# Kernel optimization log

Hardware: AMD Instinct MI355X
Metric: run time of the kernel (lower is better)

## Reference

```python
import jax, jax.numpy as jnp
import numpy as np

HID = 50        # lstm hidden_dim (hardcoded by Linear(50,100) etc.)
HS = 165        # lstm input size = 100 + 46 + 19
FEAT = 100      # encoder feature dim of H
CQ = 50257      # countq (output vocab)
EXT = 1000      # extended (copy) vocab
L = 250000      # source length


def setup_inputs() -> dict:
    key = jax.random.key(0)
    ks = jax.random.split(key, 24)
    s = 0.05
    f32 = jnp.float32
    inp = {}
    inp["H"] = jax.random.normal(ks[0], (1, L, FEAT), f32)
    inp["y"] = jax.random.normal(ks[1], (HS,), f32)
    inp["h0"] = jax.random.normal(ks[2], (1, 1, HID), f32)
    inp["c0"] = jax.random.normal(ks[3], (1, 1, HID), f32)
    inp["cont"] = jax.random.randint(ks[4], (L,), 0, CQ + EXT, dtype=jnp.int32)
    inp["ext"] = EXT
    # LSTM params (PyTorch gate order: i, f, g, o)
    inp["W_ih"] = jax.random.normal(ks[5], (4 * HID, HS), f32) * s
    inp["W_hh"] = jax.random.normal(ks[6], (4 * HID, HID), f32) * s
    inp["b_ih"] = jax.random.normal(ks[7], (4 * HID,), f32) * s
    inp["b_hh"] = jax.random.normal(ks[8], (4 * HID,), f32) * s
    # Linear layers (torch weight layout [out, in])
    inp["w_h_W"] = jax.random.normal(ks[9], (FEAT, HID), f32) * s
    inp["w_h_b"] = jax.random.normal(ks[10], (FEAT,), f32) * s
    inp["l1_W"] = jax.random.normal(ks[11], (200, 150), f32) * s
    inp["l1_b"] = jax.random.normal(ks[12], (200,), f32) * s
    inp["l2_W"] = jax.random.normal(ks[13], (CQ, 200), f32) * s
    inp["l2_b"] = jax.random.normal(ks[14], (CQ,), f32) * s
    inp["l3_W"] = jax.random.normal(ks[15], (1, HID), f32) * s
    inp["l3_b"] = jax.random.normal(ks[16], (1,), f32) * s
    inp["l4_W"] = jax.random.normal(ks[17], (1, HID), f32) * s
    inp["l4_b"] = jax.random.normal(ks[18], (1,), f32) * s
    return inp


def reference(H, y, h0, c0, cont, ext, W_ih, W_hh, b_ih, b_hh,
              w_h_W, w_h_b, l1_W, l1_b, l2_W, l2_b, l3_W, l3_b, l4_W, l4_b):
    # --- single LSTM step (batch=1, layer=1) ---
    h_prev = h0[0, 0]                       # [HID]
    c_prev = c0[0, 0]                       # [HID]
    gates = W_ih @ y + b_ih + W_hh @ h_prev + b_hh   # [4*HID]
    i, f, g, o = jnp.split(gates, 4)
    i = jax.nn.sigmoid(i); f = jax.nn.sigmoid(f)
    g = jnp.tanh(g);       o = jax.nn.sigmoid(o)
    c_new = f * c_prev + i * g
    h_new = o * jnp.tanh(c_new)             # [HID]
    # --- attention over source ---
    q = w_h_W @ h_new + w_h_b               # [FEAT]
    a_t = jax.nn.softmax(H[0] @ q)          # [L]
    c_t = H[0].T @ a_t                      # [FEAT]
    # --- vocab distribution ---
    temp = jnp.concatenate([h_new, c_t], 0)         # [150]
    e_t = jax.nn.sigmoid(l1_W @ temp + l1_b)        # [200]
    out = l2_W @ e_t + l2_b                         # [CQ]
    out = jnp.concatenate([out, jnp.zeros((ext,), out.dtype)], 0)  # [CQ+ext]
    p1 = jax.nn.sigmoid(l3_W @ h_new + l3_b)[0]     # scalar
    p2 = jax.nn.sigmoid(l4_W @ h_new + l4_b)[0]     # scalar
    out = p1 * out
    attn = p2 * a_t                                  # [L]
    # pointer copy: scatter_add attention mass into extended vocab
    out = out.at[cont].add(attn)
    logp = jax.nn.log_softmax(out)[None, :]          # [1, CQ+ext]
    return logp, h_new[None, None, :], c_new[None, None, :]
```

## Files before the change

### kernel.cpp

```cpp
#include <hip/hip_runtime.h>
#include <math.h>

#define L 250000
#define FEAT 100
#define HID 50
#define HS 165
#define CQ 50257
#define EXTV 1000
#define NOUT (CQ + EXTV)

#define NBLK23 2048
#define NW23 (NBLK23 * 4)
#define NBLK5R ((NOUT + 63) / 64)
#define NCOL 101

#define WS_Q     0
#define WS_P1    100
#define WS_P2    101
#define WS_SCALE 102
#define WS_DENOM 103
#define WS_CT    104
#define WS_ET    204
#define WS_H     404
#define WS_LSE   454
#define WS_ADD   512
#define WS_OUT   51776
#define WS_MS    103040
#define WS_PT    104960

__device__ __forceinline__ float sigm(float x) { return 1.f / (1.f + expf(-x)); }

__global__ void k1_lstm(const float* __restrict__ y, const float* __restrict__ h0,
                        const float* __restrict__ c0,
                        const float* __restrict__ W_ih, const float* __restrict__ W_hh,
                        const float* __restrict__ b_ih, const float* __restrict__ b_hh,
                        const float* __restrict__ w_h_W, const float* __restrict__ w_h_b,
                        const float* __restrict__ l3_W, const float* __restrict__ l3_b,
                        const float* __restrict__ l4_W, const float* __restrict__ l4_b,
                        float* __restrict__ ws, float* __restrict__ out) {
    int t = threadIdx.x;
    if (blockIdx.x != 0) {
        float* add = ws + WS_ADD;
        for (int i = (blockIdx.x - 1) * 256 + t; i < NOUT; i += 63 * 256) add[i] = 0.f;
        return;
    }
    __shared__ float s_y[HS], s_h[HID], s_c[HID], s_g[4 * HID], s_hn[HID];
    if (t < HS) s_y[t] = y[t];
    if (t < HID) { s_h[t] = h0[t]; s_c[t] = c0[t]; }
    __syncthreads();
    if (t < 4 * HID) {
        float acc = b_ih[t] + b_hh[t];
        const float* wi = W_ih + t * HS;
        for (int k = 0; k < HS; ++k) acc += wi[k] * s_y[k];
        const float* wh = W_hh + t * HID;
        for (int k = 0; k < HID; ++k) acc += wh[k] * s_h[k];
        s_g[t] = acc;
    }
    __syncthreads();
    if (t < HID) {
        float ig = sigm(s_g[t]);
        float fg = sigm(s_g[HID + t]);
        float gg = tanhf(s_g[2 * HID + t]);
        float og = sigm(s_g[3 * HID + t]);
        float cn = fg * s_c[t] + ig * gg;
        float hn = og * tanhf(cn);
        s_hn[t] = hn;
        ws[WS_H + t] = hn;
        out[NOUT + t] = hn;
        out[NOUT + HID + t] = cn;
    }
    __syncthreads();
    if (t < FEAT) {
        float acc = w_h_b[t];
        const float* w = w_h_W + t * HID;
        for (int k = 0; k < HID; ++k) acc += w[k] * s_hn[k];
        ws[WS_Q + t] = acc;
    }
    if (t == 200) {
        float acc = l3_b[0];
        for (int k = 0; k < HID; ++k) acc += l3_W[k] * s_hn[k];
        ws[WS_P1] = sigm(acc);
    }
    if (t == 201) {
        float acc = l4_b[0];
        for (int k = 0; k < HID; ++k) acc += l4_W[k] * s_hn[k];
        ws[WS_P2] = sigm(acc);
    }
}

__global__ void __launch_bounds__(256, 8)
k23_fused(const float* __restrict__ H, const int* __restrict__ cont,
          float* __restrict__ ws, float* __restrict__ pt) {
    __shared__ float s_ct[4][FEAT];
    __shared__ float s_d[4];
    int t = threadIdx.x;
    int w = t >> 6, lane = t & 63;
    int l32 = lane & 31, half = lane >> 5;
    long wid = (long)blockIdx.x * 4 + w;
    long r0 = (wid * L) / NW23;
    long r1 = ((wid + 1) * L) / NW23;

    float q[4];
    q[0] = ws[WS_Q + l32];
    q[1] = ws[WS_Q + l32 + 32];
    q[2] = ws[WS_Q + l32 + 64];
    q[3] = (l32 < 4) ? ws[WS_Q + l32 + 96] : 0.f;

    float cacc[4] = {0.f, 0.f, 0.f, 0.f};
    float dacc = 0.f, my_e = 0.f;

    for (long r = r0; r < r1; r += 8) {
        float hh[4][4], pd[4];
#pragma unroll
        for (int p = 0; p < 4; ++p) {
            long row = r + 2 * p + half;
            if (row < r1) {
                const float* P = H + row * FEAT;
                hh[p][0] = P[l32];
                hh[p][1] = P[l32 + 32];
                hh[p][2] = P[l32 + 64];
                hh[p][3] = (l32 < 4) ? P[l32 + 96] : 0.f;
            } else {
                hh[p][0] = hh[p][1] = hh[p][2] = hh[p][3] = 0.f;
            }
        }
#pragma unroll
        for (int p = 0; p < 4; ++p)
            pd[p] = hh[p][0] * q[0] + hh[p][1] * q[1] + hh[p][2] * q[2] + hh[p][3] * q[3];
#pragma unroll
        for (int o = 1; o < 32; o <<= 1) {
#pragma unroll
            for (int p = 0; p < 4; ++p) pd[p] += __shfl_xor(pd[p], o);
        }
#pragma unroll
        for (int p = 0; p < 4; ++p) {
            float e = expf(pd[p]);
            float eo = __shfl_xor(e, 32);
            float eA = half ? eo : e;
            float eB = half ? e : eo;
            long rA = r + 2 * p, rB = rA + 1;
            if (rA < r1) {
                dacc += eA;
                my_e = ((int)(rA - r0) == lane) ? eA : my_e;
            }
            if (rB < r1) {
                dacc += eB;
                my_e = ((int)(rB - r0) == lane) ? eB : my_e;
            }
            cacc[0] += e * hh[p][0];
            cacc[1] += e * hh[p][1];
            cacc[2] += e * hh[p][2];
            cacc[3] += e * hh[p][3];
        }
    }
#pragma unroll
    for (int k = 0; k < 4; ++k) cacc[k] += __shfl_xor(cacc[k], 32);
    int cnt = (int)(r1 - r0);
    if (lane < cnt) {
        int c = cont[r0 + lane];
        atomicAdd(ws + WS_ADD + c, my_e);
    }
    if (half == 0) {
        s_ct[w][l32] = cacc[0];
        s_ct[w][l32 + 32] = cacc[1];
        s_ct[w][l32 + 64] = cacc[2];
        if (l32 < 4) s_ct[w][96 + l32] = cacc[3];
    }
    if (lane == 0) s_d[w] = dacc;
    __syncthreads();
    if (t < FEAT)
        pt[(size_t)t * NBLK23 + blockIdx.x] =
            s_ct[0][t] + s_ct[1][t] + s_ct[2][t] + s_ct[3][t];
    if (t == FEAT)
        pt[(size_t)FEAT * NBLK23 + blockIdx.x] = s_d[0] + s_d[1] + s_d[2] + s_d[3];
}

__global__ void k3r_reduce(const float* __restrict__ pt, float* __restrict__ ws) {
    __shared__ float sw[4];
    int col = blockIdx.x;
    int t = threadIdx.x;
    const float* p = pt + (size_t)col * NBLK23;
    float s = 0.f;
#pragma unroll
    for (int k = 0; k < NBLK23 / 256; ++k) s += p[t + k * 256];
#pragma unroll
    for (int o = 1; o < 64; o <<= 1) s += __shfl_xor(s, o);
    if ((t & 63) == 0) sw[t >> 6] = s;
    __syncthreads();
    if (t == 0) {
        float tot = sw[0] + sw[1] + sw[2] + sw[3];
        if (col < FEAT) ws[WS_CT + col] = tot;
        else ws[WS_DENOM] = tot;
    }
}

__global__ void k4_et(const float* __restrict__ l1_W, const float* __restrict__ l1_b,
                      float* __restrict__ ws) {
    __shared__ float s_t[152];
    int t = threadIdx.x;
    float denom = ws[WS_DENOM];
    if (t < HID) s_t[t] = ws[WS_H + t];
    if (t < FEAT) s_t[HID + t] = ws[WS_CT + t] / denom;
    if (t == 0) ws[WS_SCALE] = ws[WS_P2] / denom;
    __syncthreads();
    if (t < 200) {
        float acc = l1_b[t];
        const float* wv = l1_W + t * 150;
        for (int k = 0; k < 150; ++k) acc += wv[k] * s_t[k];
        ws[WS_ET + t] = sigm(acc);
    }
}

__global__ void __launch_bounds__(256)
k5_vocab(const float* __restrict__ l2_W, const float* __restrict__ l2_b,
         float* __restrict__ ws, float* __restrict__ outv) {
    __shared__ float4 s_e[50];
    __shared__ float s_ms[8];
    int t = threadIdx.x, w = t >> 6, lane = t & 63;
    if (t < 50) s_e[t] = ((const float4*)(ws + WS_ET))[t];
    __syncthreads();
    float p1 = ws[WS_P1], scale = ws[WS_SCALE];
    const float* add = ws + WS_ADD;
    int row = blockIdx.x * 64 + (t >> 2);
    int q = t & 3;
    float m = -1e30f, s = 0.f;
    float acc = 0.f;
    if (row < CQ) {
        const float4* wrow = (const float4*)l2_W + (size_t)row * 50;
        float4 a[13];
#pragma unroll
        for (int j = 0; j < 12; ++j) a[j] = wrow[q + 4 * j];
        a[12] = (q < 2) ? wrow[48 + q] : make_float4(0.f, 0.f, 0.f, 0.f);
#pragma unroll
        for (int j = 0; j < 12; ++j) {
            float4 b = s_e[q + 4 * j];
            acc += a[j].x * b.x + a[j].y * b.y + a[j].z * b.z + a[j].w * b.w;
        }
        if (q < 2) {
            float4 b = s_e[48 + q];
            acc += a[12].x * b.x + a[12].y * b.y + a[12].z * b.z + a[12].w * b.w;
        }
    }
    acc += __shfl_xor(acc, 1);
    acc += __shfl_xor(acc, 2);
    if (q == 0 && row < NOUT) {
        float val = (row < CQ) ? p1 * (acc + l2_b[row]) + scale * add[row]
                               : scale * add[row];
        outv[row] = val;
        m = val; s = 1.f;
    }
#pragma unroll
    for (int o = 1; o < 64; o <<= 1) {
        float mb = __shfl_xor(m, o), sb = __shfl_xor(s, o);
        float mn = fmaxf(m, mb);
        s = s * expf(m - mn) + sb * expf(mb - mn);
        m = mn;
    }
    if (lane == 0) { s_ms[w * 2] = m; s_ms[w * 2 + 1] = s; }
    __syncthreads();
    if (t == 0) {
        float mg = s_ms[0], sg = s_ms[1];
        for (int k = 1; k < 4; ++k) {
            float mb = s_ms[2 * k], sb = s_ms[2 * k + 1];
            float mn = fmaxf(mg, mb);
            sg = sg * expf(mg - mn) + sb * expf(mb - mn);
            mg = mn;
        }
        ws[WS_MS + 2 * blockIdx.x] = mg;
        ws[WS_MS + 2 * blockIdx.x + 1] = sg;
    }
}

__global__ void k6_lse(float* __restrict__ ws) {
    __shared__ float s_ms[8];
    int t = threadIdx.x, w = t >> 6, lane = t & 63;
    const float* msbuf = ws + WS_MS;
    float mg = -1e30f, sg = 0.f;
    for (int k = t; k < NBLK5R; k += 256) {
        float mb = msbuf[2 * k], sb = msbuf[2 * k + 1];
        float mn = fmaxf(mg, mb);
        sg = sg * expf(mg - mn) + sb * expf(mb - mn);
        mg = mn;
    }
#pragma unroll
    for (int o = 1; o < 64; o <<= 1) {
        float mb = __shfl_xor(mg, o), sb = __shfl_xor(sg, o);
        float mn = fmaxf(mg, mb);
        sg = sg * expf(mg - mn) + sb * expf(mb - mn);
        mg = mn;
    }
    if (lane == 0) { s_ms[w * 2] = mg; s_ms[w * 2 + 1] = sg; }
    __syncthreads();
    if (t == 0) {
        float M = s_ms[0], S = s_ms[1];
        for (int k = 1; k < 4; ++k) {
            float mb = s_ms[2 * k], sb = s_ms[2 * k + 1];
            float mn = fmaxf(M, mb);
            S = S * expf(M - mn) + sb * expf(mb - mn);
            M = mn;
        }
        ws[WS_LSE] = M + logf(S);
    }
}

__global__ void k7c_final(const float* __restrict__ outv, const float* __restrict__ ws,
                          float* __restrict__ dout) {
    float lse = ws[WS_LSE];
    int j = blockIdx.x * blockDim.x + threadIdx.x;
    if (j < NOUT) dout[j] = outv[j] - lse;
}

extern "C" void kernel_launch(void* const* d_in, const int* in_sizes, int n_in,
                              void* d_out, int out_size, void* d_ws, size_t ws_size,
                              hipStream_t stream) {
    const float* H    = (const float*)d_in[0];
    const float* y    = (const float*)d_in[1];
    const float* h0   = (const float*)d_in[2];
    const float* c0   = (const float*)d_in[3];
    const int*   cont = (const int*)d_in[4];
    const float* W_ih = (const float*)d_in[6];
    const float* W_hh = (const float*)d_in[7];
    const float* b_ih = (const float*)d_in[8];
    const float* b_hh = (const float*)d_in[9];
    const float* w_h_W = (const float*)d_in[10];
    const float* w_h_b = (const float*)d_in[11];
    const float* l1_W = (const float*)d_in[12];
    const float* l1_b = (const float*)d_in[13];
    const float* l2_W = (const float*)d_in[14];
    const float* l2_b = (const float*)d_in[15];
    const float* l3_W = (const float*)d_in[16];
    const float* l3_b = (const float*)d_in[17];
    const float* l4_W = (const float*)d_in[18];
    const float* l4_b = (const float*)d_in[19];

    float* ws  = (float*)d_ws;
    float* out = (float*)d_out;

    k1_lstm<<<64, 256, 0, stream>>>(y, h0, c0, W_ih, W_hh, b_ih, b_hh,
                                    w_h_W, w_h_b, l3_W, l3_b, l4_W, l4_b, ws, out);

    k23_fused<<<NBLK23, 256, 0, stream>>>(H, cont, ws, ws + WS_PT);

    k3r_reduce<<<NCOL, 256, 0, stream>>>(ws + WS_PT, ws);

    k4_et<<<1, 256, 0, stream>>>(l1_W, l1_b, ws);

    k5_vocab<<<NBLK5R, 256, 0, stream>>>(l2_W, l2_b, ws, ws + WS_OUT);

    k6_lse<<<1, 256, 0, stream>>>(ws);

    k7c_final<<<(NOUT + 255) / 256, 256, 0, stream>>>(ws + WS_OUT, ws, out);
}
```

Before: 67.27 us.

## Fuse e_t computation into vocab kernel and LSE into final kernel

Removes two single-block launches by recomputing the 200-element e_t layer redundantly in every vocab block and recomputing the global log-sum-exp over per-block partials in every final-output block. This removes launch gaps and serialized tiny kernels in the dependency chain. The cost is redundant work: each of ~800 vocab blocks rereads l1_W (120KB, likely cached) and each of ~200 final blocks re-reduces ~800 partials.

```diff
diff --git a/kernel.cpp b/kernel.cpp
--- a/kernel.cpp
+++ b/kernel.cpp
@@ -17,12 +17,9 @@
 #define WS_Q     0
 #define WS_P1    100
 #define WS_P2    101
-#define WS_SCALE 102
 #define WS_DENOM 103
 #define WS_CT    104
-#define WS_ET    204
 #define WS_H     404
-#define WS_LSE   454
 #define WS_ADD   512
 #define WS_OUT   51776
 #define WS_MS    103040
@@ -194,32 +191,26 @@
     }
 }
 
-__global__ void k4_et(const float* __restrict__ l1_W, const float* __restrict__ l1_b,
-                      float* __restrict__ ws) {
+__global__ void __launch_bounds__(256)
+k5_vocab(const float* __restrict__ l1_W, const float* __restrict__ l1_b,
+         const float* __restrict__ l2_W, const float* __restrict__ l2_b,
+         float* __restrict__ ws, float* __restrict__ outv) {
+    __shared__ float4 s_e[50];
     __shared__ float s_t[152];
-    int t = threadIdx.x;
+    __shared__ float s_ms[8];
+    int t = threadIdx.x, w = t >> 6, lane = t & 63;
     float denom = ws[WS_DENOM];
     if (t < HID) s_t[t] = ws[WS_H + t];
     if (t < FEAT) s_t[HID + t] = ws[WS_CT + t] / denom;
-    if (t == 0) ws[WS_SCALE] = ws[WS_P2] / denom;
     __syncthreads();
     if (t < 200) {
         float acc = l1_b[t];
         const float* wv = l1_W + t * 150;
         for (int k = 0; k < 150; ++k) acc += wv[k] * s_t[k];
-        ws[WS_ET + t] = sigm(acc);
-    }
-}
-
-__global__ void __launch_bounds__(256)
-k5_vocab(const float* __restrict__ l2_W, const float* __restrict__ l2_b,
-         float* __restrict__ ws, float* __restrict__ outv) {
-    __shared__ float4 s_e[50];
-    __shared__ float s_ms[8];
-    int t = threadIdx.x, w = t >> 6, lane = t & 63;
-    if (t < 50) s_e[t] = ((const float4*)(ws + WS_ET))[t];
-    __syncthreads();
-    float p1 = ws[WS_P1], scale = ws[WS_SCALE];
+        ((float*)s_e)[t] = sigm(acc);
+    }
+    __syncthreads();
+    float p1 = ws[WS_P1], scale = ws[WS_P2] / denom;
     const float* add = ws + WS_ADD;
     int row = blockIdx.x * 64 + (t >> 2);
     int q = t & 3;
@@ -271,8 +262,11 @@
     }
 }
 
-__global__ void k6_lse(float* __restrict__ ws) {
+__global__ void __launch_bounds__(256)
+k7c_final(const float* __restrict__ outv, const float* __restrict__ ws,
+          float* __restrict__ dout) {
     __shared__ float s_ms[8];
+    __shared__ float s_lse;
     int t = threadIdx.x, w = t >> 6, lane = t & 63;
     const float* msbuf = ws + WS_MS;
     float mg = -1e30f, sg = 0.f;
@@ -299,15 +293,11 @@
             S = S * expf(M - mn) + sb * expf(mb - mn);
             M = mn;
         }
-        ws[WS_LSE] = M + logf(S);
-    }
-}
-
-__global__ void k7c_final(const float* __restrict__ outv, const float* __restrict__ ws,
-                          float* __restrict__ dout) {
-    float lse = ws[WS_LSE];
-    int j = blockIdx.x * blockDim.x + threadIdx.x;
-    if (j < NOUT) dout[j] = outv[j] - lse;
+        s_lse = M + logf(S);
+    }
+    __syncthreads();
+    int j = blockIdx.x * 256 + t;
+    if (j < NOUT) dout[j] = outv[j] - s_lse;
 }
 
 extern "C" void kernel_launch(void* const* d_in, const int* in_sizes, int n_in,
@@ -343,11 +333,7 @@
 
     k3r_reduce<<<NCOL, 256, 0, stream>>>(ws + WS_PT, ws);
 
-    k4_et<<<1, 256, 0, stream>>>(l1_W, l1_b, ws);
-
-    k5_vocab<<<NBLK5R, 256, 0, stream>>>(l2_W, l2_b, ws, ws + WS_OUT);
-
-    k6_lse<<<1, 256, 0, stream>>>(ws);
+    k5_vocab<<<NBLK5R, 256, 0, stream>>>(l1_W, l1_b, l2_W, l2_b, ws, ws + WS_OUT);
 
     k7c_final<<<(NOUT + 255) / 256, 256, 0, stream>>>(ws + WS_OUT, ws, out);
 }
```

After: 69.54 us. 3.4% more time.
